# Optimization experiments

Measured on AMD Instinct MI355X. Metric: run time of the kernel, lower is better.

Reference implementation:

```python
import jax, jax.numpy as jnp
from jax import lax
import numpy as np

B, L, W = 32, 128, 16
CHAR_VOCAB, CHAR_EMBED = 100, 64
NUM_FILTERS, KERNEL = 128, 3
WORD_VOCAB, WORD_EMBED = 50000, 256
EMBED = NUM_FILTERS + WORD_EMBED  # 384
HIDDEN = 512
OUT_SIZE = 512
NUM_CLASSES = 17


def setup_inputs() -> dict:
    key = jax.random.key(0)
    ks = jax.random.split(key, 16)
    s = 0.05
    char_emb = jax.random.normal(ks[0], (CHAR_VOCAB, CHAR_EMBED), jnp.float32) * s
    char_emb = char_emb.at[0].set(0.0)  # padding_idx=0
    word_emb = jax.random.normal(ks[1], (WORD_VOCAB, WORD_EMBED), jnp.float32) * s
    conv_w = jax.random.normal(ks[2], (NUM_FILTERS, CHAR_EMBED, KERNEL), jnp.float32) * s
    conv_b = jnp.zeros((NUM_FILTERS,), jnp.float32)
    G = 4 * HIDDEN
    w_ih_f = jax.random.normal(ks[3], (G, EMBED), jnp.float32) * s
    w_hh_f = jax.random.normal(ks[4], (G, HIDDEN), jnp.float32) * s
    b_f = jax.random.normal(ks[5], (G,), jnp.float32) * s
    w_ih_b = jax.random.normal(ks[6], (G, EMBED), jnp.float32) * s
    w_hh_b = jax.random.normal(ks[7], (G, HIDDEN), jnp.float32) * s
    b_b = jax.random.normal(ks[8], (G,), jnp.float32) * s
    w1 = jax.random.normal(ks[9], (OUT_SIZE, 2 * HIDDEN), jnp.float32) * s
    b1 = jnp.zeros((OUT_SIZE,), jnp.float32)
    w2 = jax.random.normal(ks[10], (NUM_CLASSES, OUT_SIZE), jnp.float32) * s
    b2 = jnp.zeros((NUM_CLASSES,), jnp.float32)
    word_ids = jax.random.randint(ks[11], (B, L), 0, WORD_VOCAB, jnp.int32)
    char_ids = jax.random.randint(ks[12], (B, L, W), 0, CHAR_VOCAB, jnp.int32)
    mask = jnp.ones((B, L), jnp.bool_)
    return dict(word_ids=word_ids, char_ids=char_ids, mask=mask,
                char_emb=char_emb, word_emb=word_emb, conv_w=conv_w, conv_b=conv_b,
                w_ih_f=w_ih_f, w_hh_f=w_hh_f, b_f=b_f,
                w_ih_b=w_ih_b, w_hh_b=w_hh_b, b_b=b_b,
                w1=w1, b1=b1, w2=w2, b2=b2)


def _lstm_scan(xs, w_ih, w_hh, b):
    # xs: [L, B, E] -> hs: [L, B, H]; PyTorch gate order i,f,g,o
    H = w_hh.shape[1]
    gates_x = jnp.einsum('lbe,ge->lbg', xs, w_ih) + b  # precompute input projection

    def step(carry, gx):
        h, c = carry
        gates = gx + h @ w_hh.T
        i, f, g, o = jnp.split(gates, 4, axis=-1)
        c = jax.nn.sigmoid(f) * c + jax.nn.sigmoid(i) * jnp.tanh(g)
        h = jax.nn.sigmoid(o) * jnp.tanh(c)
        return (h, c), h

    nB = xs.shape[1]
    init = (jnp.zeros((nB, H), xs.dtype), jnp.zeros((nB, H), xs.dtype))
    _, hs = lax.scan(step, init, gates_x)
    return hs


def reference(word_ids, char_ids, mask, char_emb, word_emb, conv_w, conv_b,
              w_ih_f, w_hh_f, b_f, w_ih_b, w_hh_b, b_b, w1, b1, w2, b2):
    Bb, Ll, Ww = char_ids.shape
    # char CNN
    ce = char_emb[char_ids.reshape(Bb * Ll, Ww)]         # [BL, W, Cc]
    ce = ce.transpose(0, 2, 1)                           # [BL, Cc, W]
    pad = conv_w.shape[2] // 2
    y = lax.conv_general_dilated(ce, conv_w, (1,), [(pad, pad)],
                                 dimension_numbers=('NCH', 'OIH', 'NCH'))
    y = jax.nn.relu(y + conv_b[None, :, None])           # [BL, F, W]
    char_x = y.max(axis=2).reshape(Bb, Ll, -1)           # [B, L, F]
    # word embedding + concat
    x = jnp.concatenate([char_x, word_emb[word_ids]], axis=-1)  # [B, L, E]
    # bidirectional LSTM (dropout is identity in eval)
    xs = x.transpose(1, 0, 2)                            # [L, B, E]
    hf = _lstm_scan(xs, w_ih_f, w_hh_f, b_f)
    hb = _lstm_scan(xs[::-1], w_ih_b, w_hh_b, b_b)[::-1]
    h = jnp.concatenate([hf, hb], axis=-1).transpose(1, 0, 2)  # [B, L, 2H]
    # head: Linear -> ELU -> Linear
    z = jax.nn.elu(h @ w1.T + b1)
    return z @ w2.T + b2                                 # [B, L, num_classes]
```

## Files before the change

kernel.cpp:

```cpp
#include <hip/hip_runtime.h>
#include <math.h>

#define B_   32
#define L_   128
#define W_   16
#define CE_  64
#define NF_  128
#define WE_  256
#define E_   384
#define H_   512
#define G4_  2048
#define O1_  512
#define NC_  17
#define LSTM_BLOCKS 64
#define AGENT_SC __HIP_MEMORY_SCOPE_AGENT

typedef __attribute__((ext_vector_type(4))) float f32x4;
typedef _Float16 half8 __attribute__((ext_vector_type(8)));
typedef _Float16 half4 __attribute__((ext_vector_type(4)));

__device__ inline half8 cvt8(float4 a, float4 b) {
    half8 r;
    r[0] = (_Float16)a.x; r[1] = (_Float16)a.y;
    r[2] = (_Float16)a.z; r[3] = (_Float16)a.w;
    r[4] = (_Float16)b.x; r[5] = (_Float16)b.y;
    r[6] = (_Float16)b.z; r[7] = (_Float16)b.w;
    return r;
}

__device__ inline unsigned int ld_u32_sc1(const unsigned int* p) {
    unsigned int v;
    asm volatile("global_load_dword %0, %1, off sc1\n\ts_waitcnt vmcnt(0)"
                 : "=v"(v) : "v"(p) : "memory");
    return v;
}
__device__ inline half8 ld_b128_sc1(const void* p) {
    half8 v;
    asm volatile("global_load_dwordx4 %0, %1, off sc1"
                 : "=v"(v) : "v"(p) : "memory");
    return v;
}

__device__ inline float sigm_f(float x) { return 1.f / (1.f + __expf(-x)); }
__device__ inline float tanh_f(float x) { return 2.f / (1.f + __expf(-2.f * x)) - 1.f; }

__global__ __launch_bounds__(256) void conv_transpose_k(
    const float* __restrict__ cw, float* __restrict__ cwT)
{
    int i = blockIdx.x * 256 + threadIdx.x;
    int f = i / 192;
    int rem = i - f * 192;
    int c = rem / 3;
    int k = rem - c * 3;
    cwT[(c * 3 + k) * NF_ + f] = cw[i];
}

__global__ __launch_bounds__(64) void embed_cnn(
    const int* __restrict__ word_ids, const int* __restrict__ char_ids,
    const float* __restrict__ char_emb, const float* __restrict__ word_emb,
    const float* __restrict__ cwT, const float* __restrict__ conv_b,
    _Float16* __restrict__ x_h)
{
    __shared__ float ce[CE_][20];
    __shared__ int ids[W_];
    int bl = blockIdx.x;
    int tid = threadIdx.x;

    if (tid < W_) ids[tid] = char_ids[bl * W_ + tid];
    ce[tid][0] = 0.f;
    ce[tid][17] = 0.f;
    __syncthreads();

    for (int i = tid; i < W_ * CE_; i += 64) {
        int w = i >> 6, c = i & 63;
        ce[c][w + 1] = char_emb[ids[w] * CE_ + c];
    }
    __syncthreads();

    int f0 = tid, f1 = tid + 64;
    float acc0[W_], acc1[W_];
#pragma unroll
    for (int w = 0; w < W_; w++) { acc0[w] = 0.f; acc1[w] = 0.f; }

    for (int c = 0; c < CE_; c++) {
        float win[18];
        float4 v0 = *(const float4*)&ce[c][0];
        float4 v1 = *(const float4*)&ce[c][4];
        float4 v2 = *(const float4*)&ce[c][8];
        float4 v3 = *(const float4*)&ce[c][12];
        win[0]=v0.x; win[1]=v0.y; win[2]=v0.z; win[3]=v0.w;
        win[4]=v1.x; win[5]=v1.y; win[6]=v1.z; win[7]=v1.w;
        win[8]=v2.x; win[9]=v2.y; win[10]=v2.z; win[11]=v2.w;
        win[12]=v3.x; win[13]=v3.y; win[14]=v3.z; win[15]=v3.w;
        win[16] = ce[c][16];
        win[17] = ce[c][17];
        const float* wp = cwT + c * 3 * NF_;
        float k00 = wp[f0], k01 = wp[NF_ + f0], k02 = wp[2 * NF_ + f0];
        float k10 = wp[f1], k11 = wp[NF_ + f1], k12 = wp[2 * NF_ + f1];
#pragma unroll
        for (int w = 0; w < W_; w++) {
            acc0[w] += win[w] * k00 + win[w + 1] * k01 + win[w + 2] * k02;
            acc1[w] += win[w] * k10 + win[w + 1] * k11 + win[w + 2] * k12;
        }
    }
    float m0 = acc0[0], m1 = acc1[0];
#pragma unroll
    for (int w = 1; w < W_; w++) { m0 = fmaxf(m0, acc0[w]); m1 = fmaxf(m1, acc1[w]); }
    m0 = fmaxf(0.f, m0 + conv_b[f0]);
    m1 = fmaxf(0.f, m1 + conv_b[f1]);
    x_h[bl * E_ + f0] = (_Float16)m0;
    x_h[bl * E_ + f1] = (_Float16)m1;

    int wid = word_ids[bl];
    float4 wv = *(const float4*)&word_emb[wid * WE_ + tid * 4];
    half4 h;
    h[0] = (_Float16)wv.x; h[1] = (_Float16)wv.y;
    h[2] = (_Float16)wv.z; h[3] = (_Float16)wv.w;
    *(half4*)&x_h[bl * E_ + NF_ + tid * 4] = h;
}

__device__ __forceinline__ void gemm_f16_body(
    const _Float16* A, const float* Wt, const float* bias, void* C,
    int bm, int bn, int N, int K, int mode, int act, int fp16out)
{
    __shared__ _Float16 As[64 * 32];
    __shared__ _Float16 Bs[64 * 32];
    int tid = threadIdx.x;
    int l = tid & 63;
    int mt = tid >> 6;
    int lr = l & 15, lk = l >> 4;

    int srow = tid >> 2, skq = (tid & 3) << 3;
    int sbyteA = ((srow * 64 + skq * 2) ^ ((srow & 7) << 4));

    f32x4 d[4] = {{0.f,0.f,0.f,0.f},{0.f,0.f,0.f,0.f},
                  {0.f,0.f,0.f,0.f},{0.f,0.f,0.f,0.f}};

    for (int kt = 0; kt < K; kt += 32) {
        half8 av = *(const half8*)&A[(size_t)(bm + srow) * K + kt + skq];
        const float* wp = &Wt[(size_t)(bn + srow) * K + kt + skq];
        float4 w0 = *(const float4*)wp;
        float4 w1 = *(const float4*)(wp + 4);
        *(half8*)((char*)As + sbyteA) = av;
        *(half8*)((char*)Bs + sbyteA) = cvt8(w0, w1);
        __syncthreads();

        int arow = mt * 16 + lr;
        half8 af = *(const half8*)((char*)As +
                     ((arow * 64 + lk * 16) ^ ((arow & 7) << 4)));
#pragma unroll
        for (int nt = 0; nt < 4; nt++) {
            int brow = nt * 16 + lr;
            half8 bf = *(const half8*)((char*)Bs +
                         ((brow * 64 + lk * 16) ^ ((brow & 7) << 4)));
            d[nt] = __builtin_amdgcn_mfma_f32_16x16x32_f16(af, bf, d[nt], 0, 0, 0);
        }
        __syncthreads();
    }

#pragma unroll
    for (int nt = 0; nt < 4; nt++) {
        int n = bn + nt * 16 + lr;
        float bv = bias[n];
#pragma unroll
        for (int r = 0; r < 4; r++) {
            int m = bm + mt * 16 + lk * 4 + r;
            int orow;
            if (mode == 0) orow = m;
            else {
                int bb = m >> 7, ll = m & 127;
                if (mode == 2) ll = 127 - ll;
                orow = ll * B_ + bb;
            }
            float v = d[nt][r] + bv;
            if (act) v = v > 0.f ? v : expm1f(v);
            if (fp16out) ((_Float16*)C)[(size_t)orow * N + n] = (_Float16)v;
            else         ((float*)C)[(size_t)orow * N + n] = v;
        }
    }
}

__global__ __launch_bounds__(256) void gemm_f16(
    const _Float16* __restrict__ A, const float* __restrict__ Wt,
    const float* __restrict__ bias, void* __restrict__ C,
    int N, int K, int mode, int act, int fp16out)
{
    gemm_f16_body(A, Wt, bias, C, blockIdx.x * 64, blockIdx.y * 64,
                  N, K, mode, act, fp16out);
}

__global__ __launch_bounds__(256) void gemm_f16_proj(
    const _Float16* __restrict__ A,
    const float* __restrict__ Wf, const float* __restrict__ Wb,
    const float* __restrict__ bf, const float* __restrict__ bb,
    float* __restrict__ gxf, float* __restrict__ gxb)
{
    int bng = blockIdx.y * 64;
    int dir = bng >> 11;
    int bn  = bng & 2047;
    gemm_f16_body(A, dir ? Wb : Wf, dir ? bb : bf,
                  dir ? (void*)gxb : (void*)gxf,
                  blockIdx.x * 64, bn, G4_, E_, 1 + dir, 0, 0);
}

__global__ __launch_bounds__(256) void gemm_bias_act(
    const float* __restrict__ A, const float* __restrict__ Wt,
    const float* __restrict__ bias, float* __restrict__ C,
    int M, int N, int K)
{
    __shared__ float As[16][68];
    __shared__ float Bs[16][68];
    int tid = threadIdx.x;
    int bm = blockIdx.x * 64;
    int bn = blockIdx.y * 64;
    int tx = tid & 15, ty = tid >> 4;
    int r = tid >> 2, kq = (tid & 3) << 2;
    float acc[4][4] = {};

    for (int kt = 0; kt < K; kt += 16) {
        float4 av = *(const float4*)&A[(bm + r) * K + kt + kq];
        As[kq + 0][r] = av.x; As[kq + 1][r] = av.y;
        As[kq + 2][r] = av.z; As[kq + 3][r] = av.w;
        int n = bn + r;
        float4 wv = make_float4(0.f, 0.f, 0.f, 0.f);
        if (n < N) wv = *(const float4*)&Wt[n * K + kt + kq];
        Bs[kq + 0][r] = wv.x; Bs[kq + 1][r] = wv.y;
        Bs[kq + 2][r] = wv.z; Bs[kq + 3][r] = wv.w;
        __syncthreads();
#pragma unroll
        for (int k = 0; k < 16; k++) {
            float4 a = *(const float4*)&As[k][ty << 2];
            float4 b = *(const float4*)&Bs[k][tx << 2];
            acc[0][0] += a.x * b.x; acc[0][1] += a.x * b.y;
            acc[0][2] += a.x * b.z; acc[0][3] += a.x * b.w;
            acc[1][0] += a.y * b.x; acc[1][1] += a.y * b.y;
            acc[1][2] += a.y * b.z; acc[1][3] += a.y * b.w;
            acc[2][0] += a.z * b.x; acc[2][1] += a.z * b.y;
            acc[2][2] += a.z * b.z; acc[2][3] += a.z * b.w;
            acc[3][0] += a.w * b.x; acc[3][1] += a.w * b.y;
            acc[3][2] += a.w * b.z; acc[3][3] += a.w * b.w;
        }
        __syncthreads();
    }

#pragma unroll
    for (int ii = 0; ii < 4; ii++) {
        int m = bm + (ty << 2) + ii;
#pragma unroll
        for (int jj = 0; jj < 4; jj++) {
            int n = bn + (tx << 2) + jj;
            if (n < N) C[m * N + n] = acc[ii][jj] + bias[n];
        }
    }
}

__global__ __launch_bounds__(256) void lstm_mfma4(
    const float* __restrict__ gxf, const float* __restrict__ gxb,
    const float* __restrict__ whh_f, const float* __restrict__ whh_b,
    unsigned int* __restrict__ hbuf,
    _Float16* __restrict__ hcat_h,
    unsigned int* __restrict__ flags)
{
    __shared__ unsigned int hlds[8192];
    __shared__ float gl[4 * 32 * 17];

    int bx = blockIdx.x;
    int dir = bx >> 5;
    int U0 = (bx & 31) * 16;
    int tid = threadIdx.x;
    int g = tid >> 6;
    int l = tid & 63;
    int lr = l & 15, lk = l >> 4;

    const float* gx = dir ? gxb : gxf;

    half8 afrag[16];
    {
        const float* wrow = (dir ? whh_b : whh_f)
                          + (size_t)(g * 512 + U0 + lr) * 512 + lk * 8;
#pragma unroll
        for (int ks = 0; ks < 16; ks++) {
            float4 a = *(const float4*)(wrow + ks * 32);
            float4 b = *(const float4*)(wrow + ks * 32 + 4);
            afrag[ks] = cvt8(a, b);
        }
    }

    int uu = tid & 15, ub = tid >> 4;
    float c0 = 0.f, c1 = 0.f;
    const unsigned int* dflags = flags + dir * 32 * 32;

    for (int t = 0; t < L_; t++) {
        float gxv0[4], gxv1[4];
        {
            const float* gxt = gx + (size_t)t * B_ * G4_;
#pragma unroll
            for (int gg = 0; gg < 4; gg++) {
                gxv0[gg] = gxt[ub * G4_ + gg * H_ + U0 + uu];
                gxv1[gg] = gxt[(ub + 16) * G4_ + gg * H_ + U0 + uu];
            }
        }

        if (t > 0) {
            unsigned tgt = (unsigned)t;
            const unsigned int* fp = dflags + (tid & 31) * 32;
            while (ld_u32_sc1(fp) < tgt)
                __builtin_amdgcn_s_sleep(1);
            __builtin_amdgcn_sched_barrier(0);
        }

        {
            const char* hsrc = (const char*)(hbuf
                             + ((((t + 1) & 1) * 2 + dir) * (32 * 256)));
            half8 tmp[8];
#pragma unroll
            for (int p = 0; p < 8; p++)
                tmp[p] = ld_b128_sc1(hsrc + p * 4096 + tid * 16);
            asm volatile("s_waitcnt vmcnt(0)" ::: "memory");
            __builtin_amdgcn_sched_barrier(0);
#pragma unroll
            for (int p = 0; p < 8; p++) {
                int o = p * 4096 + tid * 16;
                int row = o >> 10;
                *(half8*)((char*)hlds + (o ^ ((row & 7) << 4))) = tmp[p];
            }
        }
        __syncthreads();

        f32x4 d0 = {0.f, 0.f, 0.f, 0.f};
        f32x4 d1 = {0.f, 0.f, 0.f, 0.f};
        const char* hb = (const char*)hlds;
        int base0 = lr * 1024 + lk * 16;
        int base1 = (16 + lr) * 1024 + lk * 16;
        int sw0 = (lr & 7) << 4;
#pragma unroll
        for (int ks = 0; ks < 16; ks++) {
            half8 b0 = *(const half8*)(hb + ((base0 + ks * 64) ^ sw0));
            half8 b1 = *(const half8*)(hb + ((base1 + ks * 64) ^ sw0));
            d0 = __builtin_amdgcn_mfma_f32_16x16x32_f16(afrag[ks], b0, d0, 0, 0, 0);
            d1 = __builtin_amdgcn_mfma_f32_16x16x32_f16(afrag[ks], b1, d1, 0, 0, 0);
        }
#pragma unroll
        for (int r = 0; r < 4; r++) {
            gl[(g * 32 + lr) * 17 + lk * 4 + r]      = d0[r];
            gl[(g * 32 + 16 + lr) * 17 + lk * 4 + r] = d1[r];
        }
        __syncthreads();

        {
            float ga0[4], ga1[4];
#pragma unroll
            for (int gg = 0; gg < 4; gg++) {
                ga0[gg] = gl[(gg * 32 + ub) * 17 + uu] + gxv0[gg];
                ga1[gg] = gl[(gg * 32 + ub + 16) * 17 + uu] + gxv1[gg];
            }
            float i0 = sigm_f(ga0[0]);
            float f0_ = sigm_f(ga0[1]);
            float g0 = tanh_f(ga0[2]);
            float o0 = sigm_f(ga0[3]);
            c0 = f0_ * c0 + i0 * g0;
            float h0 = o0 * tanh_f(c0);

            float i1 = sigm_f(ga1[0]);
            float f1_ = sigm_f(ga1[1]);
            float g1 = tanh_f(ga1[2]);
            float o1 = sigm_f(ga1[3]);
            c1 = f1_ * c1 + i1 * g1;
            float h1 = o1 * tanh_f(c1);

            int j = U0 + uu;
            int ll = dir ? (L_ - 1 - t) : t;
            hcat_h[((size_t)ub * L_ + ll) * (2 * H_) + dir * H_ + j]        = (_Float16)h0;
            hcat_h[((size_t)(ub + 16) * L_ + ll) * (2 * H_) + dir * H_ + j] = (_Float16)h1;

            float h0n = __shfl_xor(h0, 1);
            float h1n = __shfl_xor(h1, 1);
            if ((uu & 1) == 0) {
                union { _Float16 h[2]; unsigned u; } p0, p1;
                p0.h[0] = (_Float16)h0; p0.h[1] = (_Float16)h0n;
                p1.h[0] = (_Float16)h1; p1.h[1] = (_Float16)h1n;
                unsigned int* hdst = hbuf + (((t & 1) * 2 + dir) * (32 * 256));
                int wj = (U0 + uu) >> 1;
                __hip_atomic_store(&hdst[ub * 256 + wj], p0.u,
                                   __ATOMIC_RELAXED, AGENT_SC);
                __hip_atomic_store(&hdst[(ub + 16) * 256 + wj], p1.u,
                                   __ATOMIC_RELAXED, AGENT_SC);
            }
        }

        __syncthreads();
        if (tid == 0)
            __hip_atomic_store(flags + bx * 32, (unsigned)(t + 1),
                               __ATOMIC_RELAXED, AGENT_SC);
    }
}

extern "C" void kernel_launch(void* const* d_in, const int* in_sizes, int n_in,
                              void* d_out, int out_size, void* d_ws, size_t ws_size,
                              hipStream_t stream)
{
    const int*   word_ids = (const int*)d_in[0];
    const int*   char_ids = (const int*)d_in[1];
    const float* char_emb = (const float*)d_in[3];
    const float* word_emb = (const float*)d_in[4];
    const float* conv_w   = (const float*)d_in[5];
    const float* conv_b   = (const float*)d_in[6];
    const float* w_ih_f   = (const float*)d_in[7];
    const float* w_hh_f   = (const float*)d_in[8];
    const float* b_f      = (const float*)d_in[9];
    const float* w_ih_b   = (const float*)d_in[10];
    const float* w_hh_b   = (const float*)d_in[11];
    const float* b_b      = (const float*)d_in[12];
    const float* w1       = (const float*)d_in[13];
    const float* b1       = (const float*)d_in[14];
    const float* w2       = (const float*)d_in[15];
    const float* b2       = (const float*)d_in[16];
    float* out = (float*)d_out;
    float* ws  = (float*)d_ws;

    _Float16* x_h   = (_Float16*)(ws + 0);
    float* gxf  = ws + 786432;
    float* gxb  = ws + 9175040;
    _Float16* hcat_h = (_Float16*)(ws + 17563648);
    float* z    = ws + 19660800;
    unsigned int* hbuf = (unsigned int*)(ws + 21757952);
    float* cwT  = ws + 21823488;
    unsigned int* flags = (unsigned int*)(ws + 21848064);

    hipMemsetAsync(hbuf, 0, 2 * 2 * 32 * 256 * sizeof(unsigned int), stream);
    hipMemsetAsync(flags, 0, 64 * 32 * sizeof(unsigned int), stream);

    conv_transpose_k<<<96, 256, 0, stream>>>(conv_w, cwT);
    embed_cnn<<<4096, 64, 0, stream>>>(word_ids, char_ids, char_emb, word_emb,
                                       cwT, conv_b, x_h);

    dim3 gp(64, 64);
    gemm_f16_proj<<<gp, 256, 0, stream>>>(x_h, w_ih_f, w_ih_b, b_f, b_b,
                                          gxf, gxb);

    {
        const float* a0 = gxf; const float* a1 = gxb;
        const float* a2 = w_hh_f; const float* a3 = w_hh_b;
        unsigned int* a4 = hbuf;
        _Float16* a5 = hcat_h;
        unsigned int* a6 = flags;
        void* args[] = { &a0, &a1, &a2, &a3, &a4, &a5, &a6 };
        hipLaunchCooperativeKernel((void*)lstm_mfma4, dim3(LSTM_BLOCKS), dim3(256),
                                   args, 0, stream);
    }

    dim3 g2(64, 8);
    gemm_f16<<<g2, 256, 0, stream>>>(hcat_h, w1, b1, z, O1_, 2 * H_, 0, 1, 0);
    dim3 g3(64, 1);
    gemm_bias_act<<<g3, 256, 0, stream>>>(z, w2, b2, out, 4096, NC_, O1_);
}
```

Baseline: 666.0 us.

## Rewrite GEMMs with 128x128 tiles, pre-converted fp16 weights, and register-only LSTM gates

A prep kernel converts the input-projection and head weights to fp16 once, transposes the conv weights, and zeroes the flags, replacing two memsets and the conv-transpose kernel. The projection and head GEMMs use 128x128 tiles with direct global-to-LDS loads and 4x4 MFMA fragments per wave. The embedding writes rows in time-major order, which simplifies the output index mapping. The LSTM reorders the recurrent weight rows so each lane's MFMA accumulator holds all four gates of one unit. This removes the LDS gate exchange and a barrier per step, skips the h load at t=0, and writes hcat as packed pairs. The unswizzled LDS layout in the new GEMM may cause bank conflicts, and the hbuf memset is dropped.

```diff
diff --git a/kernel.cpp b/kernel.cpp
--- a/kernel.cpp
+++ b/kernel.cpp
@@ -44,15 +44,33 @@
 __device__ inline float sigm_f(float x) { return 1.f / (1.f + __expf(-x)); }
 __device__ inline float tanh_f(float x) { return 2.f / (1.f + __expf(-2.f * x)) - 1.f; }
 
-__global__ __launch_bounds__(256) void conv_transpose_k(
-    const float* __restrict__ cw, float* __restrict__ cwT)
+__global__ __launch_bounds__(256) void prep_k(
+    const float* __restrict__ wf, const float* __restrict__ wb,
+    const float* __restrict__ w1, const float* __restrict__ cw,
+    _Float16* __restrict__ w16, float* __restrict__ cwT,
+    unsigned int* __restrict__ flags)
 {
     int i = blockIdx.x * 256 + threadIdx.x;
-    int f = i / 192;
-    int rem = i - f * 192;
-    int c = rem / 3;
-    int k = rem - c * 3;
-    cwT[(c * 3 + k) * NF_ + f] = cw[i];
+    if (i < 524288) {
+        const float* src; _Float16* dst; int j;
+        if (i < 196608)      { src = wf; dst = w16;           j = i; }
+        else if (i < 393216) { src = wb; dst = w16 + 786432;  j = i - 196608; }
+        else                 { src = w1; dst = w16 + 1572864; j = i - 393216; }
+        float4 v = ((const float4*)src)[j];
+        half4 h;
+        h[0] = (_Float16)v.x; h[1] = (_Float16)v.y;
+        h[2] = (_Float16)v.z; h[3] = (_Float16)v.w;
+        ((half4*)dst)[j] = h;
+    } else if (i < 548864) {
+        int t = i - 524288;
+        int f = t / 192;
+        int rem = t - f * 192;
+        int c = rem / 3;
+        int k = rem - c * 3;
+        cwT[(c * 3 + k) * NF_ + f] = cw[t];
+    } else {
+        flags[i - 548864] = 0;
+    }
 }
 
 __global__ __launch_bounds__(64) void embed_cnn(
@@ -65,6 +83,7 @@
     __shared__ int ids[W_];
     int bl = blockIdx.x;
     int tid = threadIdx.x;
+    int orow = ((bl & 127) << 5) | (bl >> 7);
 
     if (tid < W_) ids[tid] = char_ids[bl * W_ + tid];
     ce[tid][0] = 0.f;
@@ -108,99 +127,106 @@
     for (int w = 1; w < W_; w++) { m0 = fmaxf(m0, acc0[w]); m1 = fmaxf(m1, acc1[w]); }
     m0 = fmaxf(0.f, m0 + conv_b[f0]);
     m1 = fmaxf(0.f, m1 + conv_b[f1]);
-    x_h[bl * E_ + f0] = (_Float16)m0;
-    x_h[bl * E_ + f1] = (_Float16)m1;
+    x_h[orow * E_ + f0] = (_Float16)m0;
+    x_h[orow * E_ + f1] = (_Float16)m1;
 
     int wid = word_ids[bl];
     float4 wv = *(const float4*)&word_emb[wid * WE_ + tid * 4];
     half4 h;
     h[0] = (_Float16)wv.x; h[1] = (_Float16)wv.y;
     h[2] = (_Float16)wv.z; h[3] = (_Float16)wv.w;
-    *(half4*)&x_h[bl * E_ + NF_ + tid * 4] = h;
-}
-
-__device__ __forceinline__ void gemm_f16_body(
-    const _Float16* A, const float* Wt, const float* bias, void* C,
-    int bm, int bn, int N, int K, int mode, int act, int fp16out)
-{
-    __shared__ _Float16 As[64 * 32];
-    __shared__ _Float16 Bs[64 * 32];
+    *(half4*)&x_h[orow * E_ + NF_ + tid * 4] = h;
+}
+
+__device__ __forceinline__ void gemm128_body(
+    const _Float16* A, const _Float16* Wt, const float* bias, float* C,
+    int bm, int bn, int N, int K, int mode, int act)
+{
+    __shared__ _Float16 As[128 * 32];
+    __shared__ _Float16 Bs[128 * 32];
     int tid = threadIdx.x;
-    int l = tid & 63;
-    int mt = tid >> 6;
-    int lr = l & 15, lk = l >> 4;
-
-    int srow = tid >> 2, skq = (tid & 3) << 3;
-    int sbyteA = ((srow * 64 + skq * 2) ^ ((srow & 7) << 4));
-
-    f32x4 d[4] = {{0.f,0.f,0.f,0.f},{0.f,0.f,0.f,0.f},
-                  {0.f,0.f,0.f,0.f},{0.f,0.f,0.f,0.f}};
+    int wid = tid >> 6, lane = tid & 63;
+    int lr = lane & 15, lk = lane >> 4;
+    int wr = wid >> 1, wc = wid & 1;
+
+    f32x4 acc[4][4];
+#pragma unroll
+    for (int mi = 0; mi < 4; mi++)
+#pragma unroll
+        for (int ni = 0; ni < 4; ni++)
+            acc[mi][ni] = (f32x4){0.f, 0.f, 0.f, 0.f};
+
+    int srow = wid * 32 + (lane >> 2);
+    int kb   = (lane & 3) * 16;
 
     for (int kt = 0; kt < K; kt += 32) {
-        half8 av = *(const half8*)&A[(size_t)(bm + srow) * K + kt + skq];
-        const float* wp = &Wt[(size_t)(bn + srow) * K + kt + skq];
-        float4 w0 = *(const float4*)wp;
-        float4 w1 = *(const float4*)(wp + 4);
-        *(half8*)((char*)As + sbyteA) = av;
-        *(half8*)((char*)Bs + sbyteA) = cvt8(w0, w1);
+        const char* Ab = (const char*)A + ((size_t)bm * K + kt) * 2;
+        const char* Bb = (const char*)Wt + ((size_t)bn * K + kt) * 2;
+#pragma unroll
+        for (int inst = 0; inst < 2; inst++) {
+            int row = srow + inst * 16;
+            int lb  = wid * 2048 + inst * 1024;
+            __builtin_amdgcn_global_load_lds(
+                (const __attribute__((address_space(1))) void*)(Ab + (size_t)row * (K * 2) + kb),
+                (__attribute__((address_space(3))) void*)((char*)As + lb), 16, 0, 0);
+            __builtin_amdgcn_global_load_lds(
+                (const __attribute__((address_space(1))) void*)(Bb + (size_t)row * (K * 2) + kb),
+                (__attribute__((address_space(3))) void*)((char*)Bs + lb), 16, 0, 0);
+        }
         __syncthreads();
 
-        int arow = mt * 16 + lr;
-        half8 af = *(const half8*)((char*)As +
-                     ((arow * 64 + lk * 16) ^ ((arow & 7) << 4)));
-#pragma unroll
-        for (int nt = 0; nt < 4; nt++) {
-            int brow = nt * 16 + lr;
-            half8 bf = *(const half8*)((char*)Bs +
-                         ((brow * 64 + lk * 16) ^ ((brow & 7) << 4)));
-            d[nt] = __builtin_amdgcn_mfma_f32_16x16x32_f16(af, bf, d[nt], 0, 0, 0);
-        }
+        half8 af[4], bf[4];
+#pragma unroll
+        for (int mi = 0; mi < 4; mi++)
+            af[mi] = *(const half8*)((const char*)As + (wr * 64 + mi * 16 + lr) * 64 + lk * 16);
+#pragma unroll
+        for (int ni = 0; ni < 4; ni++)
+            bf[ni] = *(const half8*)((const char*)Bs + (wc * 64 + ni * 16 + lr) * 64 + lk * 16);
+#pragma unroll
+        for (int mi = 0; mi < 4; mi++)
+#pragma unroll
+            for (int ni = 0; ni < 4; ni++)
+                acc[mi][ni] = __builtin_amdgcn_mfma_f32_16x16x32_f16(
+                                  af[mi], bf[ni], acc[mi][ni], 0, 0, 0);
         __syncthreads();
     }
 
 #pragma unroll
-    for (int nt = 0; nt < 4; nt++) {
-        int n = bn + nt * 16 + lr;
+    for (int ni = 0; ni < 4; ni++) {
+        int n = bn + wc * 64 + ni * 16 + lr;
         float bv = bias[n];
 #pragma unroll
-        for (int r = 0; r < 4; r++) {
-            int m = bm + mt * 16 + lk * 4 + r;
-            int orow;
-            if (mode == 0) orow = m;
-            else {
-                int bb = m >> 7, ll = m & 127;
-                if (mode == 2) ll = 127 - ll;
-                orow = ll * B_ + bb;
+        for (int mi = 0; mi < 4; mi++) {
+#pragma unroll
+            for (int r = 0; r < 4; r++) {
+                int m = bm + wr * 64 + mi * 16 + lk * 4 + r;
+                int orow = m;
+                if (mode == 2) orow = ((127 - (m >> 5)) << 5) | (m & 31);
+                float v = acc[mi][ni][r] + bv;
+                if (act) v = v > 0.f ? v : expm1f(v);
+                C[(size_t)orow * N + n] = v;
             }
-            float v = d[nt][r] + bv;
-            if (act) v = v > 0.f ? v : expm1f(v);
-            if (fp16out) ((_Float16*)C)[(size_t)orow * N + n] = (_Float16)v;
-            else         ((float*)C)[(size_t)orow * N + n] = v;
-        }
-    }
-}
-
-__global__ __launch_bounds__(256) void gemm_f16(
-    const _Float16* __restrict__ A, const float* __restrict__ Wt,
-    const float* __restrict__ bias, void* __restrict__ C,
-    int N, int K, int mode, int act, int fp16out)
-{
-    gemm_f16_body(A, Wt, bias, C, blockIdx.x * 64, blockIdx.y * 64,
-                  N, K, mode, act, fp16out);
-}
-
-__global__ __launch_bounds__(256) void gemm_f16_proj(
-    const _Float16* __restrict__ A,
-    const float* __restrict__ Wf, const float* __restrict__ Wb,
+        }
+    }
+}
+
+__global__ __launch_bounds__(256) void gemm128_proj(
+    const _Float16* __restrict__ x16, const _Float16* __restrict__ w16,
     const float* __restrict__ bf, const float* __restrict__ bb,
     float* __restrict__ gxf, float* __restrict__ gxb)
 {
-    int bng = blockIdx.y * 64;
-    int dir = bng >> 11;
-    int bn  = bng & 2047;
-    gemm_f16_body(A, dir ? Wb : Wf, dir ? bb : bf,
-                  dir ? (void*)gxb : (void*)gxf,
-                  blockIdx.x * 64, bn, G4_, E_, 1 + dir, 0, 0);
+    int dir = blockIdx.z;
+    gemm128_body(x16, w16 + (size_t)dir * 786432, dir ? bb : bf,
+                 dir ? gxb : gxf, blockIdx.x * 128, blockIdx.y * 128,
+                 G4_, E_, 1 + dir, 0);
+}
+
+__global__ __launch_bounds__(256) void gemm128_head(
+    const _Float16* __restrict__ hcat16, const _Float16* __restrict__ w116,
+    const float* __restrict__ b1, float* __restrict__ z)
+{
+    gemm128_body(hcat16, w116, b1, z, blockIdx.x * 128, blockIdx.y * 128,
+                 O1_, 2 * H_, 0, 1);
 }
 
 __global__ __launch_bounds__(256) void gemm_bias_act(
@@ -254,7 +280,7 @@
     }
 }
 
-__global__ __launch_bounds__(256) void lstm_mfma4(
+__global__ __launch_bounds__(256) void lstm_mfma5(
     const float* __restrict__ gxf, const float* __restrict__ gxb,
     const float* __restrict__ whh_f, const float* __restrict__ whh_b,
     unsigned int* __restrict__ hbuf,
@@ -262,22 +288,23 @@
     unsigned int* __restrict__ flags)
 {
     __shared__ unsigned int hlds[8192];
-    __shared__ float gl[4 * 32 * 17];
 
     int bx = blockIdx.x;
     int dir = bx >> 5;
     int U0 = (bx & 31) * 16;
     int tid = threadIdx.x;
-    int g = tid >> 6;
-    int l = tid & 63;
-    int lr = l & 15, lk = l >> 4;
+    int wid = tid >> 6;
+    int lane = tid & 63;
+    int lr = lane & 15, lk = lane >> 4;
 
     const float* gx = dir ? gxb : gxf;
 
     half8 afrag[16];
     {
+        int ua = U0 + wid * 4 + (lr >> 2);
+        int gg = lr & 3;
         const float* wrow = (dir ? whh_b : whh_f)
-                          + (size_t)(g * 512 + U0 + lr) * 512 + lk * 8;
+                          + (size_t)(gg * H_ + ua) * H_ + lk * 8;
 #pragma unroll
         for (int ks = 0; ks < 16; ks++) {
             float4 a = *(const float4*)(wrow + ks * 32);
@@ -286,7 +313,8 @@
         }
     }
 
-    int uu = tid & 15, ub = tid >> 4;
+    int b0 = lr, b1 = lr + 16;
+    int u = U0 + wid * 4 + lk;
     float c0 = 0.f, c1 = 0.f;
     const unsigned int* dflags = flags + dir * 32 * 32;
 
@@ -296,95 +324,83 @@
             const float* gxt = gx + (size_t)t * B_ * G4_;
 #pragma unroll
             for (int gg = 0; gg < 4; gg++) {
-                gxv0[gg] = gxt[ub * G4_ + gg * H_ + U0 + uu];
-                gxv1[gg] = gxt[(ub + 16) * G4_ + gg * H_ + U0 + uu];
+                gxv0[gg] = gxt[b0 * G4_ + gg * H_ + u];
+                gxv1[gg] = gxt[b1 * G4_ + gg * H_ + u];
             }
         }
 
+        f32x4 d0 = {0.f, 0.f, 0.f, 0.f};
+        f32x4 d1 = {0.f, 0.f, 0.f, 0.f};
         if (t > 0) {
             unsigned tgt = (unsigned)t;
             const unsigned int* fp = dflags + (tid & 31) * 32;
             while (ld_u32_sc1(fp) < tgt)
                 __builtin_amdgcn_s_sleep(1);
             __builtin_amdgcn_sched_barrier(0);
+
+            {
+                const char* hsrc = (const char*)(hbuf
+                                 + ((((t + 1) & 1) * 2 + dir) * (32 * 256)));
+                half8 tmp[8];
+#pragma unroll
+                for (int p = 0; p < 8; p++)
+                    tmp[p] = ld_b128_sc1(hsrc + p * 4096 + tid * 16);
+                asm volatile("s_waitcnt vmcnt(0)" ::: "memory");
+                __builtin_amdgcn_sched_barrier(0);
+#pragma unroll
+                for (int p = 0; p < 8; p++) {
+                    int o = p * 4096 + tid * 16;
+                    int row = o >> 10;
+                    *(half8*)((char*)hlds + (o ^ ((row & 7) << 4))) = tmp[p];
+                }
+            }
+            __syncthreads();
+
+            const char* hb = (const char*)hlds;
+            int base0 = lr * 1024 + lk * 16;
+            int base1 = (16 + lr) * 1024 + lk * 16;
+            int sw = (lr & 7) << 4;
+#pragma unroll
+            for (int ks = 0; ks < 16; ks++) {
+                half8 f0 = *(const half8*)(hb + ((base0 + ks * 64) ^ sw));
+                half8 f1 = *(const half8*)(hb + ((base1 + ks * 64) ^ sw));
+                d0 = __builtin_amdgcn_mfma_f32_16x16x32_f16(afrag[ks], f0, d0, 0, 0, 0);
+                d1 = __builtin_amdgcn_mfma_f32_16x16x32_f16(afrag[ks], f1, d1, 0, 0, 0);
+            }
         }
 
         {
-            const char* hsrc = (const char*)(hbuf
-                             + ((((t + 1) & 1) * 2 + dir) * (32 * 256)));
-            half8 tmp[8];
-#pragma unroll
-            for (int p = 0; p < 8; p++)
-                tmp[p] = ld_b128_sc1(hsrc + p * 4096 + tid * 16);
-            asm volatile("s_waitcnt vmcnt(0)" ::: "memory");
-            __builtin_amdgcn_sched_barrier(0);
-#pragma unroll
-            for (int p = 0; p < 8; p++) {
-                int o = p * 4096 + tid * 16;
-                int row = o >> 10;
-                *(half8*)((char*)hlds + (o ^ ((row & 7) << 4))) = tmp[p];
-            }
-        }
-        __syncthreads();
-
-        f32x4 d0 = {0.f, 0.f, 0.f, 0.f};
-        f32x4 d1 = {0.f, 0.f, 0.f, 0.f};
-        const char* hb = (const char*)hlds;
-        int base0 = lr * 1024 + lk * 16;
-        int base1 = (16 + lr) * 1024 + lk * 16;
-        int sw0 = (lr & 7) << 4;
-#pragma unroll
-        for (int ks = 0; ks < 16; ks++) {
-            half8 b0 = *(const half8*)(hb + ((base0 + ks * 64) ^ sw0));
-            half8 b1 = *(const half8*)(hb + ((base1 + ks * 64) ^ sw0));
-            d0 = __builtin_amdgcn_mfma_f32_16x16x32_f16(afrag[ks], b0, d0, 0, 0, 0);
-            d1 = __builtin_amdgcn_mfma_f32_16x16x32_f16(afrag[ks], b1, d1, 0, 0, 0);
-        }
-#pragma unroll
-        for (int r = 0; r < 4; r++) {
-            gl[(g * 32 + lr) * 17 + lk * 4 + r]      = d0[r];
-            gl[(g * 32 + 16 + lr) * 17 + lk * 4 + r] = d1[r];
-        }
-        __syncthreads();
-
-        {
-            float ga0[4], ga1[4];
-#pragma unroll
-            for (int gg = 0; gg < 4; gg++) {
-                ga0[gg] = gl[(gg * 32 + ub) * 17 + uu] + gxv0[gg];
-                ga1[gg] = gl[(gg * 32 + ub + 16) * 17 + uu] + gxv1[gg];
-            }
-            float i0 = sigm_f(ga0[0]);
-            float f0_ = sigm_f(ga0[1]);
-            float g0 = tanh_f(ga0[2]);
-            float o0 = sigm_f(ga0[3]);
+            float i0 = sigm_f(d0[0] + gxv0[0]);
+            float f0_ = sigm_f(d0[1] + gxv0[1]);
+            float g0 = tanh_f(d0[2] + gxv0[2]);
+            float o0 = sigm_f(d0[3] + gxv0[3]);
             c0 = f0_ * c0 + i0 * g0;
             float h0 = o0 * tanh_f(c0);
 
-            float i1 = sigm_f(ga1[0]);
-            float f1_ = sigm_f(ga1[1]);
-            float g1 = tanh_f(ga1[2]);
-            float o1 = sigm_f(ga1[3]);
+            float i1 = sigm_f(d1[0] + gxv1[0]);
+            float f1_ = sigm_f(d1[1] + gxv1[1]);
+            float g1 = tanh_f(d1[2] + gxv1[2]);
+            float o1 = sigm_f(d1[3] + gxv1[3]);
             c1 = f1_ * c1 + i1 * g1;
             float h1 = o1 * tanh_f(c1);
 
-            int j = U0 + uu;
+            float h0n = __shfl_xor(h0, 16);
+            float h1n = __shfl_xor(h1, 16);
             int ll = dir ? (L_ - 1 - t) : t;
-            hcat_h[((size_t)ub * L_ + ll) * (2 * H_) + dir * H_ + j]        = (_Float16)h0;
-            hcat_h[((size_t)(ub + 16) * L_ + ll) * (2 * H_) + dir * H_ + j] = (_Float16)h1;
-
-            float h0n = __shfl_xor(h0, 1);
-            float h1n = __shfl_xor(h1, 1);
-            if ((uu & 1) == 0) {
-                union { _Float16 h[2]; unsigned u; } p0, p1;
+            if ((lk & 1) == 0) {
+                union { _Float16 h[2]; unsigned v; } p0, p1;
                 p0.h[0] = (_Float16)h0; p0.h[1] = (_Float16)h0n;
                 p1.h[0] = (_Float16)h1; p1.h[1] = (_Float16)h1n;
                 unsigned int* hdst = hbuf + (((t & 1) * 2 + dir) * (32 * 256));
-                int wj = (U0 + uu) >> 1;
-                __hip_atomic_store(&hdst[ub * 256 + wj], p0.u,
+                int wj = u >> 1;
+                __hip_atomic_store(&hdst[b0 * 256 + wj], p0.v,
                                    __ATOMIC_RELAXED, AGENT_SC);
-                __hip_atomic_store(&hdst[(ub + 16) * 256 + wj], p1.u,
+                __hip_atomic_store(&hdst[b1 * 256 + wj], p1.v,
                                    __ATOMIC_RELAXED, AGENT_SC);
+                *(unsigned int*)((char*)hcat_h
+                    + ((size_t)(b0 * L_ + ll)) * 2048 + dir * 1024 + u * 2) = p0.v;
+                *(unsigned int*)((char*)hcat_h
+                    + ((size_t)(b1 * L_ + ll)) * 2048 + dir * 1024 + u * 2) = p1.v;
             }
         }
 
@@ -425,18 +441,15 @@
     float* z    = ws + 19660800;
     unsigned int* hbuf = (unsigned int*)(ws + 21757952);
     float* cwT  = ws + 21823488;
-    unsigned int* flags = (unsigned int*)(ws + 21848064);
-
-    hipMemsetAsync(hbuf, 0, 2 * 2 * 32 * 256 * sizeof(unsigned int), stream);
-    hipMemsetAsync(flags, 0, 64 * 32 * sizeof(unsigned int), stream);
-
-    conv_transpose_k<<<96, 256, 0, stream>>>(conv_w, cwT);
+    _Float16* w16 = (_Float16*)(ws + 21848064);
+    unsigned int* flags = (unsigned int*)(ws + 22896640);
+
+    prep_k<<<2152, 256, 0, stream>>>(w_ih_f, w_ih_b, w1, conv_w, w16, cwT, flags);
     embed_cnn<<<4096, 64, 0, stream>>>(word_ids, char_ids, char_emb, word_emb,
                                        cwT, conv_b, x_h);
 
-    dim3 gp(64, 64);
-    gemm_f16_proj<<<gp, 256, 0, stream>>>(x_h, w_ih_f, w_ih_b, b_f, b_b,
-                                          gxf, gxb);
+    dim3 gp(32, 16, 2);
+    gemm128_proj<<<gp, 256, 0, stream>>>(x_h, w16, b_f, b_b, gxf, gxb);
 
     {
         const float* a0 = gxf; const float* a1 = gxb;
@@ -445,12 +458,12 @@
         _Float16* a5 = hcat_h;
         unsigned int* a6 = flags;
         void* args[] = { &a0, &a1, &a2, &a3, &a4, &a5, &a6 };
-        hipLaunchCooperativeKernel((void*)lstm_mfma4, dim3(LSTM_BLOCKS), dim3(256),
+        hipLaunchCooperativeKernel((void*)lstm_mfma5, dim3(LSTM_BLOCKS), dim3(256),
                                    args, 0, stream);
     }
 
-    dim3 g2(64, 8);
-    gemm_f16<<<g2, 256, 0, stream>>>(hcat_h, w1, b1, z, O1_, 2 * H_, 0, 1, 0);
+    dim3 g2(32, 4);
+    gemm128_head<<<g2, 256, 0, stream>>>(hcat_h, w16 + 1572864, b1, z);
     dim3 g3(64, 1);
     gemm_bias_act<<<g3, 256, 0, stream>>>(z, w2, b2, out, 4096, NC_, O1_);
 }
```

Result: slower. 759.3 us (+14.0%).
